# Performance work log

Hardware: AMD Instinct MI355X
Metric: run time of the kernel (lower is better)

The kernel has to match this reference:

```python
import jax, jax.numpy as jnp
import numpy as np

N = 100000
E = 1250000
D = 64
EPS = 1e-12


def lgconv(x, edge_index):
    # PyG LGConv: symmetric gcn_norm WITHOUT self-loops, scatter-add to target.
    src, dst = edge_index[0], edge_index[1]
    n = x.shape[0]
    deg = jax.ops.segment_sum(jnp.ones((edge_index.shape[1],), x.dtype), dst, num_segments=n)
    dinv = jnp.where(deg > 0, jax.lax.rsqrt(jnp.maximum(deg, 1.0)) * (deg > 0), 0.0)
    dinv = jnp.where(deg > 0, deg ** -0.5, 0.0)
    norm = dinv[src] * dinv[dst]                      # [E]
    msgs = norm[:, None] * x[src]                     # [E, D]
    return jax.ops.segment_sum(msgs, dst, num_segments=n)


def l2_normalize(x):
    # torch F.normalize(dim=1): x / max(||x||_2, eps)
    nrm = jnp.sqrt(jnp.sum(x * x, axis=1, keepdims=True))
    return x / jnp.maximum(nrm, EPS)


def setup_inputs() -> dict:
    key = jax.random.key(0)
    ks = jax.random.split(key, 8)
    return {
        "init_feat": jax.random.normal(ks[0], (N, D), jnp.float32),
        "W1": jax.random.normal(ks[1], (3 * D, 128), jnp.float32) * (1.0 / np.sqrt(3 * D)),
        "b1": jnp.zeros((128,), jnp.float32),
        "W2": jax.random.normal(ks[2], (128, 3), jnp.float32) * (1.0 / np.sqrt(128)),
        "b2": jnp.zeros((3,), jnp.float32),
        "edge_index_title": jax.random.randint(ks[3], (2, E), 0, N, jnp.int32),
        "edge_index_year": jax.random.randint(ks[4], (2, E), 0, N, jnp.int32),
        "edge_index_cat": jax.random.randint(ks[5], (2, E), 0, N, jnp.int32),
    }


def reference(init_feat, W1, b1, W2, b2, edge_index_title, edge_index_year, edge_index_cat):
    x_title = init_feat
    for _ in range(2):
        x_title = lgconv(x_title, edge_index_title)
    x_title = l2_normalize(x_title)

    x_year = lgconv(init_feat, edge_index_year)
    x_year = l2_normalize(x_year)

    x_cat = init_feat
    for _ in range(3):
        x_cat = lgconv(x_cat, edge_index_cat)
    x_cat = l2_normalize(x_cat)

    x_all = jnp.concatenate([x_title, x_year, x_cat], axis=1)  # [N, 3D]
    h = jax.nn.relu(x_all @ W1 + b1)
    att = jax.nn.softmax(h @ W2 + b2, axis=1)                  # [N, 3]
    out = att[:, 0:1] * x_title + att[:, 1:2] * x_year + att[:, 2:3] * x_cat
    return out
```

## Files before the change

### kernel.cpp

```cpp
#include <hip/hip_runtime.h>


constexpr int NN = 100000;
constexpr int NE = 1250000;
constexpr int BROWS = 128;
constexpr int NB = (NN + BROWS - 1) / BROWS;
constexpr int PADB = 2048;
constexpr int PADE = NB * PADB;
constexpr int CHUNK = 8192;
constexpr int NCHUNK = (NE + CHUNK - 1) / CHUNK;
constexpr int XROW = 200;

typedef short bf16x8 __attribute__((ext_vector_type(8)));
typedef float f32x4 __attribute__((ext_vector_type(4)));

__device__ inline short f2bf(float f) {
    unsigned u = __builtin_bit_cast(unsigned, f);
    u += 0x7FFFu + ((u >> 16) & 1u);
    return (short)(u >> 16);
}
__device__ inline unsigned packbf(float a, float b) {
    return (unsigned)(unsigned short)f2bf(a) | ((unsigned)(unsigned short)f2bf(b) << 16);
}
__device__ inline float bflo(unsigned q) { return __builtin_bit_cast(float, q << 16); }
__device__ inline float bfhi(unsigned q) { return __builtin_bit_cast(float, q & 0xFFFF0000u); }

__device__ inline float dot2bf(unsigned a, unsigned b, float c) {
    float d;
    asm("v_dot2_f32_bf16 %0, %1, %2, %3" : "=v"(d) : "v"(a), "v"(b), "v"(c));
    return d;
}
constexpr unsigned SEL_LO = 0x00003F80u;
constexpr unsigned SEL_HI = 0x3F800000u;

__device__ inline void dotacc(float* acc, uint4 v, unsigned sl, unsigned sh) {
    acc[0] = dot2bf(v.x, sl, acc[0]); acc[1] = dot2bf(v.x, sh, acc[1]);
    acc[2] = dot2bf(v.y, sl, acc[2]); acc[3] = dot2bf(v.y, sh, acc[3]);
    acc[4] = dot2bf(v.z, sl, acc[4]); acc[5] = dot2bf(v.z, sh, acc[5]);
    acc[6] = dot2bf(v.w, sl, acc[6]); acc[7] = dot2bf(v.w, sh, acc[7]);
}

__global__ __launch_bounds__(256) void k_tobf(const float* __restrict__ x, unsigned short* __restrict__ o) {
    int i = blockIdx.x * 256 + threadIdx.x;
    if (i < NN * 16) {
        float4 v = ((const float4*)x)[i];
        uint2 r;
        r.x = packbf(v.x, v.y);
        r.y = packbf(v.z, v.w);
        ((uint2*)o)[i] = r;
    }
}

__global__ __launch_bounds__(256) void k_prep(const float* __restrict__ W1, short* __restrict__ W1t) {
    int idx = blockIdx.x * 256 + threadIdx.x;
    if (idx < 128 * 192) {
        int n = idx & 127, k = idx >> 7;
        W1t[n * 192 + k] = f2bf(W1[k * 128 + n]);
    }
}

__global__ __launch_bounds__(256) void k_ginit(int* __restrict__ gcur) {
    int i = blockIdx.x * 256 + threadIdx.x;
    if (i < 3 * NB) gcur[i] = (i % NB) * PADB;
}

__global__ __launch_bounds__(256) void k_bscat(const int* __restrict__ e0, const int* __restrict__ e1,
                                               const int* __restrict__ e2,
                                               int* __restrict__ gcur, int* __restrict__ gpacked) {
    __shared__ int lpack[CHUNK];
    __shared__ unsigned short lbkt[CHUNK];
    __shared__ int hist[NB];
    __shared__ int lbase[NB];
    __shared__ int lcur[NB];
    const int tid = threadIdx.x;
    const int set = blockIdx.x / NCHUNK;
    const int chunk = blockIdx.x % NCHUNK;
    const int* ei = (set == 0) ? e0 : (set == 1) ? e1 : e2;
    const int ebase = chunk * CHUNK;

    for (int b = tid; b < NB; b += 256) { hist[b] = 0; lcur[b] = 0; }
    __syncthreads();

    #pragma unroll
    for (int j = 0; j < CHUNK / 256; ++j) {
        int k = tid + j * 256;
        int e = ebase + k;
        if (e < NE) {
            int s = ei[e];
            int d = ei[NE + e];
            int b = d >> 7;
            lpack[k] = ((d & 127) << 17) | s;
            lbkt[k] = (unsigned short)b;
            atomicAdd(&hist[b], 1);
        } else {
            lbkt[k] = 0xFFFFu;
        }
    }
    __syncthreads();
    for (int b = tid; b < NB; b += 256) {
        int h = hist[b];
        if (h > 0) lbase[b] = atomicAdd(&gcur[set * NB + b], h);
    }
    __syncthreads();
    int* gp = gpacked + (size_t)set * PADE;
    #pragma unroll
    for (int j = 0; j < CHUNK / 256; ++j) {
        int k = tid + j * 256;
        unsigned short b = lbkt[k];
        if (b != 0xFFFFu) {
            int pos = lbase[b] + atomicAdd(&lcur[b], 1);
            gp[pos] = lpack[k];
        }
    }
}

__global__ __launch_bounds__(256) void k_bfin(int* __restrict__ gpacked, const int* __restrict__ gcur,
                                              int* __restrict__ cnt, float* __restrict__ dinv,
                                              uint2* __restrict__ dsel, int* __restrict__ rowstart) {
    __shared__ int win[PADB];
    __shared__ int hist[BROWS];
    __shared__ int rst[BROWS];
    __shared__ int lcur[BROWS];
    const int tid = threadIdx.x;
    const int set = blockIdx.x / NB, b = blockIdx.x % NB;
    if (tid < BROWS) { hist[tid] = 0; lcur[tid] = 0; }
    __syncthreads();

    const int base = b * PADB;
    const int n = gcur[set * NB + b] - base;
    int* gp = gpacked + (size_t)set * PADE + base;

    for (int k = tid; k < n; k += 256) {
        int p = gp[k];
        win[k] = p;
        atomicAdd(&hist[(p >> 17) & 127], 1);
    }
    __syncthreads();

    if (tid < 64) {
        int v0 = hist[tid], v1 = hist[64 + tid];
        int i0 = v0;
        #pragma unroll
        for (int off = 1; off < 64; off <<= 1) {
            int u = __shfl_up(i0, off);
            if (tid >= off) i0 += u;
        }
        int t0 = __shfl(i0, 63);
        int i1 = v1;
        #pragma unroll
        for (int off = 1; off < 64; off <<= 1) {
            int u = __shfl_up(i1, off);
            if (tid >= off) i1 += u;
        }
        rst[tid] = i0 - v0;
        rst[64 + tid] = t0 + i1 - v1;
    }
    __syncthreads();

    if (tid < BROWS) {
        int node = b * BROWS + tid;
        if (node < NN) {
            int c = hist[tid];
            float dv = (c > 0) ? (1.0f / sqrtf((float)c)) : 0.0f;
            cnt[set * NN + node] = c;
            dinv[set * NN + node] = dv;
            unsigned bf = (unsigned)(unsigned short)f2bf(dv);
            dsel[set * NN + node] = make_uint2(bf, bf << 16);
            rowstart[set * NN + node] = base + rst[tid];
        }
    }

    for (int k = tid; k < n; k += 256) {
        int p = win[k];
        int d = (p >> 17) & 127;
        int pos = rst[d] + atomicAdd(&lcur[d], 1);
        gp[pos] = p & 0x1FFFF;
    }
}

struct GA {
    const unsigned short* x;
    unsigned short* y;
    const int* csr;
    const int* row;
    const int* cnt;
    const float* dinv;
    const uint2* dsel;
    int sq;
};

__global__ __launch_bounds__(256) void k_gather3(GA g0, GA g1, GA g2, int perset) {
    const int bset = blockIdx.x / perset;
    const int blk = blockIdx.x - bset * perset;
    const GA ga = (bset == 0) ? g0 : (bset == 1) ? g1 : g2;
    const int node = blk * 4 + (threadIdx.x >> 6);
    const int lane = threadIdx.x & 63;
    const int slot = lane >> 3, fo = lane & 7;
    const int n = ga.cnt[node];
    float acc[8] = {0.f, 0.f, 0.f, 0.f, 0.f, 0.f, 0.f, 0.f};

    if (n > 0) {
        const int* lst = ga.csr + ga.row[node];
        if (ga.dsel == nullptr) {
            const unsigned sl = SEL_LO, sh = SEL_HI;
            int i = slot;
            for (; i + 8 < n; i += 16) {
                int s0 = lst[i], s1 = lst[i + 8];
                uint4 v0 = *(const uint4*)(ga.x + (size_t)s0 * 64 + fo * 8);
                uint4 v1 = *(const uint4*)(ga.x + (size_t)s1 * 64 + fo * 8);
                dotacc(acc, v0, sl, sh);
                dotacc(acc, v1, sl, sh);
            }
            if (i < n) {
                int s = lst[i];
                uint4 v = *(const uint4*)(ga.x + (size_t)s * 64 + fo * 8);
                dotacc(acc, v, sl, sh);
            }
        } else {
            const uint2* ds = ga.dsel;
            int i = slot;
            for (; i + 8 < n; i += 16) {
                int s0 = lst[i], s1 = lst[i + 8];
                uint2 w0 = ds[s0], w1 = ds[s1];
                uint4 v0 = *(const uint4*)(ga.x + (size_t)s0 * 64 + fo * 8);
                uint4 v1 = *(const uint4*)(ga.x + (size_t)s1 * 64 + fo * 8);
                dotacc(acc, v0, w0.x, w0.y);
                dotacc(acc, v1, w1.x, w1.y);
            }
            if (i < n) {
                int s = lst[i];
                uint2 w = ds[s];
                uint4 v = *(const uint4*)(ga.x + (size_t)s * 64 + fo * 8);
                dotacc(acc, v, w.x, w.y);
            }
        }
    }

    #pragma unroll
    for (int off = 8; off < 64; off <<= 1) {
        #pragma unroll
        for (int j = 0; j < 8; ++j) acc[j] += __shfl_xor(acc[j], off);
    }
    if (slot == 0) {
        float dn = ga.dinv[node];
        float sc = ga.sq ? dn * dn : dn;
        uint4 r;
        r.x = packbf(sc * acc[0], sc * acc[1]);
        r.y = packbf(sc * acc[2], sc * acc[3]);
        r.z = packbf(sc * acc[4], sc * acc[5]);
        r.w = packbf(sc * acc[6], sc * acc[7]);
        *(uint4*)(ga.y + (size_t)node * 64 + fo * 8) = r;
    }
}

__global__ __launch_bounds__(256) void k_final(const unsigned short* __restrict__ xt,
                                               const unsigned short* __restrict__ xy,
                                               const unsigned short* __restrict__ xc,
                                               const short* __restrict__ W1t,
                                               const float* __restrict__ b1,
                                               const float* __restrict__ W2,
                                               const float* __restrict__ b2,
                                               float* __restrict__ out) {
    __shared__ alignas(16) short Xn[64 * XROW];
    __shared__ float rnorm[3 * 64];
    __shared__ float attw[64][4];
    const int tid = threadIdx.x;
    const int wid = tid >> 6, lane = tid & 63;
    const int slot = lane >> 3, fo = lane & 7;
    const int m0 = wid * 16;
    const int nbase = blockIdx.x * 64;

    #pragma unroll
    for (int it = 0; it < 6; ++it) {
        int idx = it * 8 + slot;
        int br = idx >> 4, noff = idx & 15;
        int m = m0 + noff;
        int nodeg = nbase + m;
        const unsigned short* xp = (br == 0) ? xt : (br == 1) ? xy : xc;
        float f[8] = {0.f, 0.f, 0.f, 0.f, 0.f, 0.f, 0.f, 0.f};
        if (nodeg < NN) {
            uint4 v = *(const uint4*)(xp + (size_t)nodeg * 64 + fo * 8);
            f[0] = bflo(v.x); f[1] = bfhi(v.x); f[2] = bflo(v.y); f[3] = bfhi(v.y);
            f[4] = bflo(v.z); f[5] = bfhi(v.z); f[6] = bflo(v.w); f[7] = bfhi(v.w);
        }
        float ss = 0.f;
        #pragma unroll
        for (int j = 0; j < 8; ++j) ss = fmaf(f[j], f[j], ss);
        #pragma unroll
        for (int off = 1; off < 8; off <<= 1) ss += __shfl_xor(ss, off);
        float rn = 1.0f / fmaxf(sqrtf(ss), 1e-12f);
        uint4 r;
        r.x = packbf(f[0] * rn, f[1] * rn);
        r.y = packbf(f[2] * rn, f[3] * rn);
        r.z = packbf(f[4] * rn, f[5] * rn);
        r.w = packbf(f[6] * rn, f[7] * rn);
        *(uint4*)&Xn[m * XROW + br * 64 + fo * 8] = r;
        if (fo == 0) rnorm[br * 64 + m] = rn;
    }
    __syncthreads();

    const int mrow = lane & 15, g = lane >> 4;
    bf16x8 afr[6];
    #pragma unroll
    for (int kk = 0; kk < 6; ++kk)
        afr[kk] = *(const bf16x8*)&Xn[(m0 + mrow) * XROW + kk * 32 + g * 8];
    f32x4 acc[8];
    #pragma unroll
    for (int nt = 0; nt < 8; ++nt) acc[nt] = (f32x4){0.f, 0.f, 0.f, 0.f};
    #pragma unroll
    for (int nt = 0; nt < 8; ++nt) {
        const short* wp = W1t + (nt * 16 + mrow) * 192 + g * 8;
        #pragma unroll
        for (int kk = 0; kk < 6; ++kk)
            acc[nt] = __builtin_amdgcn_mfma_f32_16x16x32_bf16(
                afr[kk], *(const bf16x8*)(wp + kk * 32), acc[nt], 0, 0, 0);
    }
    float p[4][3] = {};
    #pragma unroll
    for (int nt = 0; nt < 8; ++nt) {
        int col = nt * 16 + mrow;
        float b1v = b1[col];
        float w20 = W2[col * 3 + 0], w21 = W2[col * 3 + 1], w22 = W2[col * 3 + 2];
        #pragma unroll
        for (int i = 0; i < 4; ++i) {
            float h = fmaxf(acc[nt][i] + b1v, 0.f);
            p[i][0] = fmaf(h, w20, p[i][0]);
            p[i][1] = fmaf(h, w21, p[i][1]);
            p[i][2] = fmaf(h, w22, p[i][2]);
        }
    }
    #pragma unroll
    for (int i = 0; i < 4; ++i)
        #pragma unroll
        for (int off = 8; off > 0; off >>= 1) {
            p[i][0] += __shfl_xor(p[i][0], off);
            p[i][1] += __shfl_xor(p[i][1], off);
            p[i][2] += __shfl_xor(p[i][2], off);
        }
    if (mrow == 0) {
        #pragma unroll
        for (int i = 0; i < 4; ++i) {
            int m = m0 + g * 4 + i;
            float l0 = p[i][0] + b2[0], l1 = p[i][1] + b2[1], l2 = p[i][2] + b2[2];
            float mx = fmaxf(l0, fmaxf(l1, l2));
            float e0 = __expf(l0 - mx), e1 = __expf(l1 - mx), e2 = __expf(l2 - mx);
            float inv = 1.0f / (e0 + e1 + e2);
            attw[m][0] = e0 * inv * rnorm[m];
            attw[m][1] = e1 * inv * rnorm[64 + m];
            attw[m][2] = e2 * inv * rnorm[128 + m];
        }
    }
    __syncthreads();

    #pragma unroll
    for (int it = 0; it < 2; ++it) {
        int m = m0 + it * 8 + slot;
        int nodeg = nbase + m;
        if (nodeg < NN) {
            size_t base = (size_t)nodeg * 64 + fo * 8;
            uint4 tv = *(const uint4*)(xt + base);
            uint4 yv = *(const uint4*)(xy + base);
            uint4 cv = *(const uint4*)(xc + base);
            float wt = attw[m][0], wy = attw[m][1], wc = attw[m][2];
            float4 lo4, hi4;
            lo4.x = wt * bflo(tv.x) + wy * bflo(yv.x) + wc * bflo(cv.x);
            lo4.y = wt * bfhi(tv.x) + wy * bfhi(yv.x) + wc * bfhi(cv.x);
            lo4.z = wt * bflo(tv.y) + wy * bflo(yv.y) + wc * bflo(cv.y);
            lo4.w = wt * bfhi(tv.y) + wy * bfhi(yv.y) + wc * bfhi(cv.y);
            hi4.x = wt * bflo(tv.z) + wy * bflo(yv.z) + wc * bflo(cv.z);
            hi4.y = wt * bfhi(tv.z) + wy * bfhi(yv.z) + wc * bfhi(cv.z);
            hi4.z = wt * bflo(tv.w) + wy * bflo(yv.w) + wc * bflo(cv.w);
            hi4.w = wt * bfhi(tv.w) + wy * bfhi(yv.w) + wc * bfhi(cv.w);
            *(float4*)(out + base) = lo4;
            *(float4*)(out + base + 4) = hi4;
        }
    }
}

extern "C" void kernel_launch(void* const* d_in, const int* in_sizes, int n_in,
                              void* d_out, int out_size, void* d_ws, size_t ws_size,
                              hipStream_t stream) {
    const float* init_feat = (const float*)d_in[0];
    const float* W1 = (const float*)d_in[1];
    const float* b1 = (const float*)d_in[2];
    const float* W2 = (const float*)d_in[3];
    const float* b2 = (const float*)d_in[4];
    const int* ei[3] = {(const int*)d_in[5], (const int*)d_in[6], (const int*)d_in[7]};

    unsigned short* B0 = (unsigned short*)d_ws;
    unsigned short* B1 = B0 + (size_t)NN * 64;
    unsigned short* B2 = B1 + (size_t)NN * 64;
    unsigned short* B3 = B2 + (size_t)NN * 64;
    unsigned short* B4 = B3 + (size_t)NN * 64;
    float* dinvA = (float*)(B4 + (size_t)NN * 64);
    uint2* dselA = (uint2*)(dinvA + 3 * NN);
    int* cntA = (int*)(dselA + 3 * NN);
    int* rowA = cntA + 3 * NN;
    int* gpackedA = rowA + 3 * NN;
    short* W1t = (short*)(gpackedA + (size_t)3 * PADE);
    int* gcurA = (int*)(W1t + 128 * 192);

    const int TB = 256;
    const int perset = NN / 4;
    const int finalGrid = (NN + 63) / 64;

    k_prep<<<(128 * 192 + TB - 1) / TB, TB, 0, stream>>>(W1, W1t);
    k_ginit<<<(3 * NB + TB - 1) / TB, TB, 0, stream>>>(gcurA);
    k_tobf<<<(NN * 16 + TB - 1) / TB, TB, 0, stream>>>(init_feat, B0);
    k_bscat<<<3 * NCHUNK, TB, 0, stream>>>(ei[0], ei[1], ei[2], gcurA, gpackedA);
    k_bfin<<<3 * NB, TB, 0, stream>>>(gpackedA, gcurA, cntA, dinvA, dselA, rowA);

    #define MKGA(xp, yp, s, DS, SQ) \
        GA{ (xp), (yp), gpackedA + (size_t)(s) * PADE, rowA + (s) * NN, \
            cntA + (s) * NN, dinvA + (s) * NN, (DS), (SQ) }
    {
        GA a0 = MKGA(B0, B2, 2, dselA + 2 * NN, 1);
        GA a1 = MKGA(B0, B1, 0, dselA + 0 * NN, 1);
        GA a2 = MKGA(B0, B3, 1, dselA + 1 * NN, 0);
        k_gather3<<<3 * perset, TB, 0, stream>>>(a0, a1, a2, perset);
    }
    {
        GA b0 = MKGA(B2, B0, 2, nullptr, 1);
        GA b1g = MKGA(B1, B4, 0, nullptr, 0);
        k_gather3<<<2 * perset, TB, 0, stream>>>(b0, b1g, b1g, perset);
    }
    {
        GA c0 = MKGA(B0, B1, 2, nullptr, 0);
        k_gather3<<<perset, TB, 0, stream>>>(c0, c0, c0, perset);
    }
    #undef MKGA

    k_final<<<finalGrid, TB, 0, stream>>>(B4, B3, B1, W1t, b1, W2, b2, (float*)d_out);
}
```

Before: 391.6 us.

## Embed bf16 edge weights into packed CSR entries and merge setup kernels

```diff
diff --git a/kernel.cpp b/kernel.cpp
--- a/kernel.cpp
+++ b/kernel.cpp
@@ -40,6 +40,16 @@
     acc[6] = dot2bf(v.w, sl, acc[6]); acc[7] = dot2bf(v.w, sh, acc[7]);
 }
 
+__global__ __launch_bounds__(256) void k_misc(const float* __restrict__ W1, short* __restrict__ W1t,
+                                              int* __restrict__ gcur) {
+    int idx = blockIdx.x * 256 + threadIdx.x;
+    if (idx < 128 * 192) {
+        int n = idx & 127, k = idx >> 7;
+        W1t[n * 192 + k] = f2bf(W1[k * 128 + n]);
+    }
+    if (idx < 3 * NB) gcur[idx] = (idx % NB) * PADB;
+}
+
 __global__ __launch_bounds__(256) void k_tobf(const float* __restrict__ x, unsigned short* __restrict__ o) {
     int i = blockIdx.x * 256 + threadIdx.x;
     if (i < NN * 16) {
@@ -49,19 +59,6 @@
         r.y = packbf(v.z, v.w);
         ((uint2*)o)[i] = r;
     }
-}
-
-__global__ __launch_bounds__(256) void k_prep(const float* __restrict__ W1, short* __restrict__ W1t) {
-    int idx = blockIdx.x * 256 + threadIdx.x;
-    if (idx < 128 * 192) {
-        int n = idx & 127, k = idx >> 7;
-        W1t[n * 192 + k] = f2bf(W1[k * 128 + n]);
-    }
-}
-
-__global__ __launch_bounds__(256) void k_ginit(int* __restrict__ gcur) {
-    int i = blockIdx.x * 256 + threadIdx.x;
-    if (i < 3 * NB) gcur[i] = (i % NB) * PADB;
 }
 
 __global__ __launch_bounds__(256) void k_bscat(const int* __restrict__ e0, const int* __restrict__ e1,
@@ -116,7 +113,7 @@
 
 __global__ __launch_bounds__(256) void k_bfin(int* __restrict__ gpacked, const int* __restrict__ gcur,
                                               int* __restrict__ cnt, float* __restrict__ dinv,
-                                              uint2* __restrict__ dsel, int* __restrict__ rowstart) {
+                                              int* __restrict__ rowstart) {
     __shared__ int win[PADB];
     __shared__ int hist[BROWS];
     __shared__ int rst[BROWS];
@@ -161,11 +158,8 @@
         int node = b * BROWS + tid;
         if (node < NN) {
             int c = hist[tid];
-            float dv = (c > 0) ? (1.0f / sqrtf((float)c)) : 0.0f;
             cnt[set * NN + node] = c;
-            dinv[set * NN + node] = dv;
-            unsigned bf = (unsigned)(unsigned short)f2bf(dv);
-            dsel[set * NN + node] = make_uint2(bf, bf << 16);
+            dinv[set * NN + node] = (c > 0) ? (1.0f / sqrtf((float)c)) : 0.0f;
             rowstart[set * NN + node] = base + rst[tid];
         }
     }
@@ -175,6 +169,20 @@
         int d = (p >> 17) & 127;
         int pos = rst[d] + atomicAdd(&lcur[d], 1);
         gp[pos] = p & 0x1FFFF;
+    }
+}
+
+__global__ __launch_bounds__(256) void k_wemb(int* __restrict__ gpacked, const int* __restrict__ gcur,
+                                              const float* __restrict__ dinv) {
+    const int set = blockIdx.x / NB, b = blockIdx.x % NB;
+    const int base = b * PADB;
+    const int n = gcur[set * NB + b] - base;
+    int* gp = gpacked + (size_t)set * PADE + base;
+    const float* dv = dinv + set * NN;
+    for (int k = threadIdx.x; k < n; k += 256) {
+        unsigned s = (unsigned)gp[k] & 0x1FFFFu;
+        unsigned w = (unsigned)(unsigned short)f2bf(dv[s]);
+        gp[k] = (int)((w << 17) | s);
     }
 }
 
@@ -185,8 +193,7 @@
     const int* row;
     const int* cnt;
     const float* dinv;
-    const uint2* dsel;
-    int sq;
+    int wemb, sq;
 };
 
 __global__ __launch_bounds__(256) void k_gather3(GA g0, GA g1, GA g2, int perset) {
@@ -201,37 +208,38 @@
 
     if (n > 0) {
         const int* lst = ga.csr + ga.row[node];
-        if (ga.dsel == nullptr) {
+        if (ga.wemb) {
+            int i = slot;
+            for (; i + 8 < n; i += 16) {
+                unsigned e0 = (unsigned)lst[i], e1 = (unsigned)lst[i + 8];
+                unsigned s0 = e0 & 0x1FFFFu, s1 = e1 & 0x1FFFFu;
+                unsigned w0 = e0 >> 17, w1 = e1 >> 17;
+                uint4 v0 = *(const uint4*)(ga.x + (size_t)s0 * 64 + fo * 8);
+                uint4 v1 = *(const uint4*)(ga.x + (size_t)s1 * 64 + fo * 8);
+                dotacc(acc, v0, w0, w0 << 16);
+                dotacc(acc, v1, w1, w1 << 16);
+            }
+            if (i < n) {
+                unsigned e = (unsigned)lst[i];
+                unsigned s = e & 0x1FFFFu, w = e >> 17;
+                uint4 v = *(const uint4*)(ga.x + (size_t)s * 64 + fo * 8);
+                dotacc(acc, v, w, w << 16);
+            }
+        } else {
             const unsigned sl = SEL_LO, sh = SEL_HI;
             int i = slot;
             for (; i + 8 < n; i += 16) {
-                int s0 = lst[i], s1 = lst[i + 8];
+                unsigned s0 = (unsigned)lst[i] & 0x1FFFFu;
+                unsigned s1 = (unsigned)lst[i + 8] & 0x1FFFFu;
                 uint4 v0 = *(const uint4*)(ga.x + (size_t)s0 * 64 + fo * 8);
                 uint4 v1 = *(const uint4*)(ga.x + (size_t)s1 * 64 + fo * 8);
                 dotacc(acc, v0, sl, sh);
                 dotacc(acc, v1, sl, sh);
             }
             if (i < n) {
-                int s = lst[i];
+                unsigned s = (unsigned)lst[i] & 0x1FFFFu;
                 uint4 v = *(const uint4*)(ga.x + (size_t)s * 64 + fo * 8);
                 dotacc(acc, v, sl, sh);
-            }
-        } else {
-            const uint2* ds = ga.dsel;
-            int i = slot;
-            for (; i + 8 < n; i += 16) {
-                int s0 = lst[i], s1 = lst[i + 8];
-                uint2 w0 = ds[s0], w1 = ds[s1];
-                uint4 v0 = *(const uint4*)(ga.x + (size_t)s0 * 64 + fo * 8);
-                uint4 v1 = *(const uint4*)(ga.x + (size_t)s1 * 64 + fo * 8);
-                dotacc(acc, v0, w0.x, w0.y);
-                dotacc(acc, v1, w1.x, w1.y);
-            }
-            if (i < n) {
-                int s = lst[i];
-                uint2 w = ds[s];
-                uint4 v = *(const uint4*)(ga.x + (size_t)s * 64 + fo * 8);
-                dotacc(acc, v, w.x, w.y);
             }
         }
     }
@@ -297,7 +305,6 @@
         *(uint4*)&Xn[m * XROW + br * 64 + fo * 8] = r;
         if (fo == 0) rnorm[br * 64 + m] = rn;
     }
-    __syncthreads();
 
     const int mrow = lane & 15, g = lane >> 4;
     bf16x8 afr[6];
@@ -350,7 +357,6 @@
             attw[m][2] = e2 * inv * rnorm[128 + m];
         }
     }
-    __syncthreads();
 
     #pragma unroll
     for (int it = 0; it < 2; ++it) {
@@ -393,8 +399,7 @@
     unsigned short* B3 = B2 + (size_t)NN * 64;
     unsigned short* B4 = B3 + (size_t)NN * 64;
     float* dinvA = (float*)(B4 + (size_t)NN * 64);
-    uint2* dselA = (uint2*)(dinvA + 3 * NN);
-    int* cntA = (int*)(dselA + 3 * NN);
+    int* cntA = (int*)(dinvA + 3 * NN);
     int* rowA = cntA + 3 * NN;
     int* gpackedA = rowA + 3 * NN;
     short* W1t = (short*)(gpackedA + (size_t)3 * PADE);
@@ -404,28 +409,28 @@
     const int perset = NN / 4;
     const int finalGrid = (NN + 63) / 64;
 
-    k_prep<<<(128 * 192 + TB - 1) / TB, TB, 0, stream>>>(W1, W1t);
-    k_ginit<<<(3 * NB + TB - 1) / TB, TB, 0, stream>>>(gcurA);
+    k_misc<<<(128 * 192 + TB - 1) / TB, TB, 0, stream>>>(W1, W1t, gcurA);
     k_tobf<<<(NN * 16 + TB - 1) / TB, TB, 0, stream>>>(init_feat, B0);
     k_bscat<<<3 * NCHUNK, TB, 0, stream>>>(ei[0], ei[1], ei[2], gcurA, gpackedA);
-    k_bfin<<<3 * NB, TB, 0, stream>>>(gpackedA, gcurA, cntA, dinvA, dselA, rowA);
-
-    #define MKGA(xp, yp, s, DS, SQ) \
+    k_bfin<<<3 * NB, TB, 0, stream>>>(gpackedA, gcurA, cntA, dinvA, rowA);
+    k_wemb<<<3 * NB, TB, 0, stream>>>(gpackedA, gcurA, dinvA);
+
+    #define MKGA(xp, yp, s, WE, SQ) \
         GA{ (xp), (yp), gpackedA + (size_t)(s) * PADE, rowA + (s) * NN, \
-            cntA + (s) * NN, dinvA + (s) * NN, (DS), (SQ) }
+            cntA + (s) * NN, dinvA + (s) * NN, (WE), (SQ) }
     {
-        GA a0 = MKGA(B0, B2, 2, dselA + 2 * NN, 1);
-        GA a1 = MKGA(B0, B1, 0, dselA + 0 * NN, 1);
-        GA a2 = MKGA(B0, B3, 1, dselA + 1 * NN, 0);
+        GA a0 = MKGA(B0, B2, 2, 1, 1);
+        GA a1 = MKGA(B0, B1, 0, 1, 1);
+        GA a2 = MKGA(B0, B3, 1, 1, 0);
         k_gather3<<<3 * perset, TB, 0, stream>>>(a0, a1, a2, perset);
     }
     {
-        GA b0 = MKGA(B2, B0, 2, nullptr, 1);
-        GA b1g = MKGA(B1, B4, 0, nullptr, 0);
+        GA b0 = MKGA(B2, B0, 2, 0, 1);
+        GA b1g = MKGA(B1, B4, 0, 0, 0);
         k_gather3<<<2 * perset, TB, 0, stream>>>(b0, b1g, b1g, perset);
     }
     {
-        GA c0 = MKGA(B0, B1, 2, nullptr, 0);
+        GA c0 = MKGA(B0, B1, 2, 0, 0);
         k_gather3<<<perset, TB, 0, stream>>>(c0, c0, c0, perset);
     }
     #undef MKGA
```

New measurement: 400.3 us. 1.02x slower.
